# Performance work log

Measured on AMD Instinct MI355X. Metric: run time of the kernel, lower is better.

Reference implementation:

```python
import jax, jax.numpy as jnp
import numpy as np

C = 1024
CI = 256  # in_channels // inter_ratio
BN_EPS = 1e-5


def setup_inputs() -> dict:
    key = jax.random.key(0)
    ks = jax.random.split(key, 12)
    B, H, W = 16, 64, 32
    xavier = lambda k, o, i: jax.random.uniform(k, (o, i), jnp.float32,
                                                -np.sqrt(6.0 / (o + i)), np.sqrt(6.0 / (o + i)))
    return {
        "x": jax.random.normal(ks[0], (B, C, H, W), jnp.float32),
        "theta_w": xavier(ks[1], CI, C), "theta_b": jnp.zeros((CI,), jnp.float32),
        "phi_w": xavier(ks[2], CI, C), "phi_b": jnp.zeros((CI,), jnp.float32),
        "g_w": xavier(ks[3], CI, C), "g_b": jnp.zeros((CI,), jnp.float32),
        "w_w": xavier(ks[4], C, CI), "w_b": jnp.zeros((C,), jnp.float32),
        # BatchNorm (inference-mode) params; random (not zero-init) so the block is non-trivial
        "bn_gamma": jax.random.normal(ks[5], (C,), jnp.float32) * 0.1 + 1.0,
        "bn_beta": jax.random.normal(ks[6], (C,), jnp.float32) * 0.1,
        "bn_mean": jax.random.normal(ks[7], (C,), jnp.float32) * 0.1,
        "bn_var": jax.random.uniform(ks[8], (C,), jnp.float32, 0.5, 1.5),
    }


def reference(x, theta_w, theta_b, phi_w, phi_b, g_w, g_b, w_w, w_b,
              bn_gamma, bn_beta, bn_mean, bn_var):
    B, Cc, H, W = x.shape
    N = H * W
    xf = x.reshape(B, Cc, N)  # [B, C, N]
    # 1x1 convs == channel GEMMs
    theta = jnp.einsum('oc,bcn->bno', theta_w, xf) + theta_b  # [B, N, Ci]
    phi = jnp.einsum('oc,bcn->bon', phi_w, xf) + phi_b[:, None]  # [B, Ci, N]
    g = jnp.einsum('oc,bcn->bno', g_w, xf) + g_b  # [B, N, Ci]
    attn = jax.nn.softmax(jnp.einsum('bno,bom->bnm', theta, phi), axis=-1)  # [B, N, N]
    y = jnp.einsum('bnm,bmo->bno', attn, g)  # [B, N, Ci]
    z = jnp.einsum('co,bno->bcn', w_w, y) + w_b[None, :, None]  # [B, C, N]
    inv = bn_gamma / jnp.sqrt(bn_var + BN_EPS)
    z = (z - bn_mean[None, :, None]) * inv[None, :, None] + bn_beta[None, :, None]
    return z.reshape(B, Cc, H, W) + x
```

## Files before the change

### kernel.cpp

```cpp
#include <hip/hip_runtime.h>
#include <cstdint>

#define BATCH 16
#define CH 1024
#define CIN 256
#define NSP 2048
#define BN_EPS 1e-5f

typedef _Float16 f16;
typedef f16   f16x4 __attribute__((ext_vector_type(4)));
typedef f16   f16x8 __attribute__((ext_vector_type(8)));
typedef float f32x4 __attribute__((ext_vector_type(4)));
typedef float f32x16 __attribute__((ext_vector_type(16)));

typedef __attribute__((address_space(3))) void lds_t;
typedef __attribute__((address_space(1))) const void gbl_t;

__device__ __forceinline__ void gld16(void* l, const void* g) {
    __builtin_amdgcn_global_load_lds((gbl_t*)g, (lds_t*)l, 16, 0, 0);
}

__global__ __launch_bounds__(256) void k_prep(
    const float* __restrict__ tw, const float* __restrict__ pw,
    const float* __restrict__ gw, const float* __restrict__ ww,
    const float* __restrict__ wb, const float* __restrict__ gamma,
    const float* __restrict__ beta, const float* __restrict__ mean,
    const float* __restrict__ var,
    f16* __restrict__ w_all, float* __restrict__ inv_out, float* __restrict__ off_out)
{
    int id = blockIdx.x * 256 + threadIdx.x;
    if (id < 4 * 262144) {
        int sel = id >> 18, off = id & 262143;
        const float* src = sel == 0 ? tw : sel == 1 ? pw : sel == 2 ? gw : ww;
        w_all[id] = (f16)src[off];
    } else {
        int c = id - 4 * 262144;
        if (c < CH) {
            float iv = gamma[c] * rsqrtf(var[c] + BN_EPS);
            inv_out[c] = iv;
            off_out[c] = (wb[c] - mean[c]) * iv + beta[c];
        }
    }
}

__global__ __launch_bounds__(256) void k_transpose_x(
    const float* __restrict__ x, f16* __restrict__ xT)
{
    __shared__ float tile[64 * 65];
    int t = threadIdx.x;
    int n0 = blockIdx.x * 64, c0 = blockIdx.y * 64, b = blockIdx.z;
    const float* xb = x + (size_t)b * CH * NSP;
    for (int k = 0; k < 4; ++k) {
        int id = t + 256 * k;
        int row = id >> 4, cc = id & 15;
        float4 v = *(const float4*)(xb + (size_t)(c0 + row) * NSP + n0 + cc * 4);
        tile[row * 65 + cc * 4 + 0] = v.x;
        tile[row * 65 + cc * 4 + 1] = v.y;
        tile[row * 65 + cc * 4 + 2] = v.z;
        tile[row * 65 + cc * 4 + 3] = v.w;
    }
    __syncthreads();
    f16* xTb = xT + (size_t)b * NSP * CH;
    for (int k = 0; k < 2; ++k) {
        int id = t + 256 * k;
        int n = id >> 3, c8 = id & 7;
        f16x8 o;
        #pragma unroll
        for (int j = 0; j < 8; ++j) o[j] = (f16)tile[(c8 * 8 + j) * 65 + n];
        *(f16x8*)(xTb + (size_t)(n0 + n) * CH + c0 + c8 * 8) = o;
    }
}

__global__ __launch_bounds__(256, 3) void k_qkv(
    const f16* __restrict__ xT, const f16* __restrict__ w_all,
    const float* __restrict__ tb, const float* __restrict__ pb,
    const float* __restrict__ gb,
    f16* __restrict__ theta, f16* __restrict__ phiT, f16* __restrict__ gT)
{
    __shared__ char smem[40960];
    f16* a_lds = (f16*)smem;
    f16* b_lds = (f16*)(smem + 8192);
    int t = threadIdx.x;
    int w = t >> 6, lane = t & 63, l15 = lane & 15, q = lane >> 4;
    int sw = l15 & 7;
    int n0 = blockIdx.x * 64, b = blockIdx.y, set = blockIdx.z;
    const f16* W  = w_all + (size_t)set * (CIN * CH);
    const f16* xA = xT + ((size_t)b * NSP + n0) * CH;

    int rA  = lane >> 3;
    int ccs = (lane & 7) ^ rA;

    f32x4 acc[4][4];
    #pragma unroll
    for (int i = 0; i < 4; ++i)
        #pragma unroll
        for (int j = 0; j < 4; ++j) acc[i][j] = (f32x4){0.f, 0.f, 0.f, 0.f};

    for (int it = 0; it < 16; ++it) {
        #pragma unroll
        for (int i = 0; i < 2; ++i) {
            int win = w * 2 + i;
            int n = win * 8 + rA;
            gld16((char*)a_lds + win * 1024,
                  xA + (size_t)n * CH + it * 64 + ccs * 8);
        }
        #pragma unroll
        for (int i = 0; i < 8; ++i) {
            int win = w * 8 + i;
            int o = win * 8 + rA;
            gld16((char*)b_lds + win * 1024,
                  W + (size_t)o * CH + it * 64 + ccs * 8);
        }
        __syncthreads();

        #pragma unroll
        for (int kl = 0; kl < 2; ++kl) {
            int c16 = kl * 4 + q;
            int pos = (c16 ^ sw) & 7;
            f16x8 af[4], bfr[4];
            #pragma unroll
            for (int tn = 0; tn < 4; ++tn)
                af[tn] = *(const f16x8*)(a_lds + (16 * tn + l15) * 64 + pos * 8);
            #pragma unroll
            for (int to = 0; to < 4; ++to)
                bfr[to] = *(const f16x8*)(b_lds + (64 * w + 16 * to + l15) * 64 + pos * 8);
            #pragma unroll
            for (int tn = 0; tn < 4; ++tn)
                #pragma unroll
                for (int to = 0; to < 4; ++to)
                    acc[tn][to] = __builtin_amdgcn_mfma_f32_16x16x32_f16(
                        af[tn], bfr[to], acc[tn][to], 0, 0, 0);
        }
        __syncthreads();
    }

    const float* bias = set == 0 ? tb : set == 1 ? pb : gb;
    float bv[4];
    #pragma unroll
    for (int to = 0; to < 4; ++to) bv[to] = bias[64 * w + 16 * to + l15];

    if (set < 2) {
        f16* e_lds = (f16*)smem;
        #pragma unroll
        for (int tn = 0; tn < 4; ++tn)
            #pragma unroll
            for (int to = 0; to < 4; ++to)
                #pragma unroll
                for (int r = 0; r < 4; ++r)
                    e_lds[(16 * tn + 4 * q + r) * 256 + 64 * w + 16 * to + l15] =
                        (f16)(acc[tn][to][r] + bv[to]);
        __syncthreads();
        f16* dst = (set == 0 ? theta : phiT) + ((size_t)b * NSP + n0) * CIN;
        for (int k2 = 0; k2 < 8; ++k2) {
            int id = t + 256 * k2;
            *(f16x8*)(dst + id * 8) = *(const f16x8*)(e_lds + id * 8);
        }
    } else {
        f16* e_lds = (f16*)smem;
        #pragma unroll
        for (int tn = 0; tn < 4; ++tn)
            #pragma unroll
            for (int to = 0; to < 4; ++to)
                #pragma unroll
                for (int r = 0; r < 4; ++r)
                    e_lds[(64 * w + 16 * to + l15) * 72 + 16 * tn + 4 * q + r] =
                        (f16)(acc[tn][to][r] + bv[to]);
        __syncthreads();
        f16* dst = gT + (size_t)b * CIN * NSP + n0;
        for (int k2 = 0; k2 < 8; ++k2) {
            int id = t + 256 * k2;
            int o = id >> 3, cc = id & 7;
            *(f16x8*)(dst + (size_t)o * NSP + cc * 8) = *(const f16x8*)(e_lds + o * 72 + cc * 8);
        }
    }
}

__global__ __launch_bounds__(256, 2) void k_attn(
    const f16* __restrict__ theta, const f16* __restrict__ phiT,
    const f16* __restrict__ gT, f16* __restrict__ y)
{
    __shared__ char smem[76032];
    f16* phi_lds = (f16*)smem;
    f16* g_lds   = (f16*)(smem + 32768);
    f16* p_lds   = (f16*)(smem + 65536);
    float* pmax_lds  = (float*)(smem + 74752);
    float* psum_lds  = (float*)(smem + 75264);
    float* alpha_lds = (float*)(smem + 75776);

    int t = threadIdx.x;
    int w = t >> 6, lane = t & 63;
    int l31 = lane & 31, hi = lane >> 5;
    int qh = w & 1, kh = w >> 1;
    int b = blockIdx.x, n0 = blockIdx.y * 64;

    const f16* thb  = theta + (size_t)b * NSP * CIN;
    const f16* phib = phiT + (size_t)b * NSP * CIN;
    const f16* gTb  = gT + (size_t)b * CIN * NSP;

    f16x8 th[16];
    {
        const f16* tp = thb + (size_t)(n0 + qh * 32 + l31) * CIN + 8 * hi;
        #pragma unroll
        for (int s = 0; s < 16; ++s) th[s] = *(const f16x8*)(tp + s * 16);
    }

    f32x16 acc[2][2];
    #pragma unroll
    for (int i = 0; i < 2; ++i)
        #pragma unroll
        for (int j = 0; j < 2; ++j)
            #pragma unroll
            for (int r = 0; r < 16; ++r) acc[i][j][r] = 0.f;
    float m_run = -INFINITY, l_run = 0.f;

    int p_cdst = lane & 31;
    int g_rin = lane >> 3, g_cdst = lane & 7;
    int gc8 = t & 7, grb = t >> 3;

    #define DMA_PHI(IT)                                                         \
        _Pragma("unroll")                                                       \
        for (int i_ = 0; i_ < 8; ++i_) {                                        \
            int win_ = w * 8 + i_;                                              \
            int row_ = win_ * 2 + hi;                                           \
            int cs_ = (p_cdst & 24) | ((p_cdst ^ row_) & 7);                    \
            gld16((char*)phi_lds + win_ * 1024,                                 \
                  phib + (size_t)((IT) * 64 + row_) * CIN + cs_ * 8);           \
        }
    #define DMA_G0()                                                            \
        _Pragma("unroll")                                                       \
        for (int i_ = 0; i_ < 8; ++i_) {                                        \
            int win_ = w * 8 + i_;                                              \
            int row_ = win_ * 8 + g_rin;                                        \
            int cs_ = g_cdst ^ (row_ & 7);                                      \
            gld16((char*)g_lds + win_ * 1024,                                   \
                  gTb + (size_t)row_ * NSP + cs_ * 8);                          \
        }

    DMA_PHI(0)
    DMA_G0()
    asm volatile("s_waitcnt vmcnt(0)" ::: "memory");
    __builtin_amdgcn_s_barrier();

    int srow = kh * 32 + l31;
    int qrow = qh * 32 + l31;
    int mli  = kh * 64 + qrow;

    f16x8 gr[8];

    for (int it = 0; it < 32; ++it) {
        if (it < 31) {
            #pragma unroll
            for (int j = 0; j < 8; ++j)
                gr[j] = *(const f16x8*)(gTb + (size_t)(grb + 32 * j) * NSP
                                        + (it + 1) * 64 + gc8 * 8);
        }
        __builtin_amdgcn_sched_barrier(0);

        f32x16 s0, s1;
        #pragma unroll
        for (int r = 0; r < 16; ++r) { s0[r] = 0.f; s1[r] = 0.f; }
        __builtin_amdgcn_s_setprio(1);
        #pragma unroll
        for (int s = 0; s < 8; ++s) {
            int ch0 = 2 * s + hi;
            int sl0 = (ch0 & 24) | ((ch0 ^ srow) & 7);
            f16x8 a0 = *(const f16x8*)(phi_lds + srow * 256 + sl0 * 8);
            s0 = __builtin_amdgcn_mfma_f32_32x32x16_f16(a0, th[s], s0, 0, 0, 0);
            int ch1 = 2 * (s + 8) + hi;
            int sl1 = (ch1 & 24) | ((ch1 ^ srow) & 7);
            f16x8 a1 = *(const f16x8*)(phi_lds + srow * 256 + sl1 * 8);
            s1 = __builtin_amdgcn_mfma_f32_32x32x16_f16(a1, th[s + 8], s1, 0, 0, 0);
        }
        __builtin_amdgcn_s_setprio(0);
        f32x16 sacc = s0 + s1;

        float tmax = sacc[0];
        #pragma unroll
        for (int r = 1; r < 16; ++r) tmax = fmaxf(tmax, sacc[r]);
        tmax = fmaxf(tmax, __shfl_xor(tmax, 32));
        if (lane < 32) pmax_lds[mli] = tmax;
        asm volatile("s_waitcnt lgkmcnt(0)" ::: "memory");
        __builtin_amdgcn_s_barrier();

        if (it < 31) DMA_PHI(it + 1)

        float tile_max = fmaxf(tmax, pmax_lds[mli ^ 64]);
        float mnew  = fmaxf(m_run, tile_max);
        float alpha = __expf(m_run - mnew);
        m_run = mnew;
        float rs = 0.f;
        float pv[16];
        #pragma unroll
        for (int r = 0; r < 16; ++r) {
            pv[r] = __expf(sacc[r] - mnew);
            rs += pv[r];
        }
        rs += __shfl_xor(rs, 32);
        if (lane < 32) {
            psum_lds[mli] = rs;
            if (kh == 0) alpha_lds[qrow] = alpha;
        }
        #pragma unroll
        for (int g4 = 0; g4 < 4; ++g4) {
            f16x4 pk = { (f16)pv[4*g4+0], (f16)pv[4*g4+1], (f16)pv[4*g4+2], (f16)pv[4*g4+3] };
            *(f16x4*)(p_lds + qrow * 72 + kh * 32 + 8 * g4 + 4 * hi) = pk;
        }
        asm volatile("s_waitcnt lgkmcnt(0)" ::: "memory");
        __builtin_amdgcn_s_barrier();

        l_run = l_run * alpha + rs + psum_lds[mli ^ 64];

        f32x4 av[2][4];
        float mn = 1.0f;
        #pragma unroll
        for (int Mt = 0; Mt < 2; ++Mt)
            #pragma unroll
            for (int g4 = 0; g4 < 4; ++g4) {
                av[Mt][g4] = *(const f32x4*)(alpha_lds + Mt * 32 + 8 * g4 + 4 * hi);
                mn = fminf(mn, fminf(fminf(av[Mt][g4][0], av[Mt][g4][1]),
                                     fminf(av[Mt][g4][2], av[Mt][g4][3])));
            }
        if (__any(mn < 1.0f)) {
            #pragma unroll
            for (int Mt = 0; Mt < 2; ++Mt)
                #pragma unroll
                for (int g4 = 0; g4 < 4; ++g4)
                    #pragma unroll
                    for (int rr = 0; rr < 4; ++rr) {
                        acc[Mt][0][4*g4+rr] *= av[Mt][g4][rr];
                        acc[Mt][1][4*g4+rr] *= av[Mt][g4][rr];
                    }
        }

        __builtin_amdgcn_s_setprio(1);
        #pragma unroll
        for (int ks = 0; ks < 4; ++ks) {
            f16x8 pa0 = *(const f16x8*)(p_lds + l31 * 72 + ks * 16 + 8 * hi);
            f16x8 pa1 = *(const f16x8*)(p_lds + (32 + l31) * 72 + ks * 16 + 8 * hi);
            int slot = (2 * ks + hi) ^ (l31 & 7);
            f16x8 gb0 = *(const f16x8*)(g_lds + (64 * w + l31) * 64 + slot * 8);
            f16x8 gb1 = *(const f16x8*)(g_lds + (64 * w + 32 + l31) * 64 + slot * 8);
            acc[0][0] = __builtin_amdgcn_mfma_f32_32x32x16_f16(pa0, gb0, acc[0][0], 0, 0, 0);
            acc[0][1] = __builtin_amdgcn_mfma_f32_32x32x16_f16(pa0, gb1, acc[0][1], 0, 0, 0);
            acc[1][0] = __builtin_amdgcn_mfma_f32_32x32x16_f16(pa1, gb0, acc[1][0], 0, 0, 0);
            acc[1][1] = __builtin_amdgcn_mfma_f32_32x32x16_f16(pa1, gb1, acc[1][1], 0, 0, 0);
        }
        __builtin_amdgcn_s_setprio(0);
        asm volatile("s_waitcnt lgkmcnt(0)" ::: "memory");
        __builtin_amdgcn_s_barrier();

        if (it < 31) {
            asm volatile("s_waitcnt vmcnt(8)" ::: "memory");
            #pragma unroll
            for (int j = 0; j < 8; ++j) {
                int o = grb + 32 * j;
                *(f16x8*)(g_lds + o * 64 + (gc8 ^ (o & 7)) * 8) = gr[j];
            }
            asm volatile("s_waitcnt vmcnt(0) lgkmcnt(0)" ::: "memory");
            __builtin_amdgcn_s_barrier();
        }
    }

    if (lane < 32 && kh == 0) alpha_lds[qrow] = 1.0f / l_run;
    __syncthreads();
    f16* e_lds = (f16*)smem;
    #pragma unroll
    for (int Mt = 0; Mt < 2; ++Mt)
        #pragma unroll
        for (int g4 = 0; g4 < 4; ++g4) {
            f32x4 lv = *(const f32x4*)(alpha_lds + Mt * 32 + 8 * g4 + 4 * hi);
            #pragma unroll
            for (int rr = 0; rr < 4; ++rr) {
                int q = Mt * 32 + 8 * g4 + 4 * hi + rr;
                #pragma unroll
                for (int Nt = 0; Nt < 2; ++Nt) {
                    int cin = 64 * w + Nt * 32 + l31;
                    e_lds[q * 264 + cin] = (f16)(acc[Mt][Nt][4*g4+rr] * lv[rr]);
                }
            }
        }
    __syncthreads();
    f16* dst = y + ((size_t)b * NSP + n0) * CIN;
    for (int k2 = 0; k2 < 8; ++k2) {
        int id = t + 256 * k2;
        int row = id >> 5, cc = id & 31;
        *(f16x8*)(dst + (size_t)row * CIN + cc * 8) = *(const f16x8*)(e_lds + row * 264 + cc * 8);
    }
    #undef DMA_PHI
    #undef DMA_G0
}

__global__ __launch_bounds__(256, 3) void k_out(
    const f16* __restrict__ yv, const f16* __restrict__ ww,
    const float* __restrict__ inv, const float* __restrict__ off,
    const float* __restrict__ x, float* __restrict__ out)
{
    __shared__ char smem[40960];
    f16*   a_lds = (f16*)smem;
    f16*   b_lds = (f16*)(smem + 8192);
    float* z_lds = (float*)smem;
    int t = threadIdx.x;
    int w = t >> 6, lane = t & 63, l15 = lane & 15, q = lane >> 4;
    int sw = l15 & 7;
    int n0 = blockIdx.x * 64, cb = blockIdx.y * 256, b = blockIdx.z;

    const f16* yA = yv + ((size_t)b * NSP + n0) * CIN;
    const f16* W  = ww + (size_t)cb * CIN;

    int rA  = lane >> 3;
    int ccs = (lane & 7) ^ rA;

    f32x4 acc[4][4];
    #pragma unroll
    for (int i = 0; i < 4; ++i)
        #pragma unroll
        for (int j = 0; j < 4; ++j) acc[i][j] = (f32x4){0.f, 0.f, 0.f, 0.f};

    for (int it = 0; it < 4; ++it) {
        #pragma unroll
        for (int i = 0; i < 2; ++i) {
            int win = w * 2 + i;
            int n = win * 8 + rA;
            gld16((char*)a_lds + win * 1024,
                  yA + (size_t)n * CIN + it * 64 + ccs * 8);
        }
        #pragma unroll
        for (int i = 0; i < 8; ++i) {
            int win = w * 8 + i;
            int o = win * 8 + rA;
            gld16((char*)b_lds + win * 1024,
                  W + (size_t)o * CIN + it * 64 + ccs * 8);
        }
        __syncthreads();

        #pragma unroll
        for (int kl = 0; kl < 2; ++kl) {
            int c16 = kl * 4 + q;
            int pos = (c16 ^ sw) & 7;
            f16x8 af[4], bfr[4];
            #pragma unroll
            for (int tn = 0; tn < 4; ++tn)
                af[tn] = *(const f16x8*)(a_lds + (16 * tn + l15) * 64 + pos * 8);
            #pragma unroll
            for (int to = 0; to < 4; ++to)
                bfr[to] = *(const f16x8*)(b_lds + (64 * w + 16 * to + l15) * 64 + pos * 8);
            #pragma unroll
            for (int tn = 0; tn < 4; ++tn)
                #pragma unroll
                for (int to = 0; to < 4; ++to)
                    acc[tn][to] = __builtin_amdgcn_mfma_f32_16x16x32_f16(
                        af[tn], bfr[to], acc[tn][to], 0, 0, 0);
        }
        __syncthreads();
    }

    float4 xv[4];
    #pragma unroll
    for (int k2 = 0; k2 < 4; ++k2) {
        int f = t + 256 * k2;
        int zrr = f >> 4, nn4 = f & 15;
        int c = cb + 64 * (zrr >> 4) + (zrr & 15);
        xv[k2] = *(const float4*)(x + ((size_t)b * CH + c) * NSP + n0 + nn4 * 4);
    }

    #pragma unroll
    for (int to = 0; to < 4; ++to) {
        #pragma unroll
        for (int tn = 0; tn < 4; ++tn)
            #pragma unroll
            for (int r = 0; r < 4; ++r)
                z_lds[(16 * w + l15) * 68 + 16 * tn + 4 * q + r] = acc[tn][to][r];
        __syncthreads();

        float4 nxt[4];
        if (to < 3) {
            #pragma unroll
            for (int k2 = 0; k2 < 4; ++k2) {
                int f = t + 256 * k2;
                int zrr = f >> 4, nn4 = f & 15;
                int c = cb + 64 * (zrr >> 4) + 16 * (to + 1) + (zrr & 15);
                nxt[k2] = *(const float4*)(x + ((size_t)b * CH + c) * NSP + n0 + nn4 * 4);
            }
        }

        #pragma unroll
        for (int k2 = 0; k2 < 4; ++k2) {
            int f = t + 256 * k2;
            int zrr = f >> 4, nn4 = f & 15;
            int c = cb + 64 * (zrr >> 4) + 16 * to + (zrr & 15);
            float4 z = *(const float4*)(z_lds + zrr * 68 + nn4 * 4);
            float iv = inv[c], ov = off[c];
            size_t idx = ((size_t)b * CH + c) * NSP + n0 + nn4 * 4;
            float4 o;
            o.x = z.x * iv + ov + xv[k2].x;
            o.y = z.y * iv + ov + xv[k2].y;
            o.z = z.z * iv + ov + xv[k2].z;
            o.w = z.w * iv + ov + xv[k2].w;
            *(float4*)(out + idx) = o;
        }

        if (to < 3) {
            #pragma unroll
            for (int k2 = 0; k2 < 4; ++k2) xv[k2] = nxt[k2];
            __syncthreads();
        }
    }
}

extern "C" void kernel_launch(void* const* d_in, const int* in_sizes, int n_in,
                              void* d_out, int out_size, void* d_ws, size_t ws_size,
                              hipStream_t stream)
{
    const float* x     = (const float*)d_in[0];
    const float* tw    = (const float*)d_in[1];
    const float* tb    = (const float*)d_in[2];
    const float* pw    = (const float*)d_in[3];
    const float* pb    = (const float*)d_in[4];
    const float* gw    = (const float*)d_in[5];
    const float* gb_   = (const float*)d_in[6];
    const float* ww    = (const float*)d_in[7];
    const float* wb    = (const float*)d_in[8];
    const float* gamma = (const float*)d_in[9];
    const float* beta  = (const float*)d_in[10];
    const float* mean  = (const float*)d_in[11];
    const float* var   = (const float*)d_in[12];
    float* out = (float*)d_out;

    char* ws = (char*)d_ws;
    f16* xT    = (f16*)ws;
    f16* theta = (f16*)(ws + 67108864);
    f16* phiT  = (f16*)(ws + 83886080);
    f16* gT    = (f16*)(ws + 100663296);
    f16* yv    = (f16*)(ws + 117440512);
    f16* w_all = (f16*)(ws + 134217728);
    float* inv  = (float*)(ws + 136314880);
    float* offv = (float*)(ws + 136318976);

    k_prep<<<4100, 256, 0, stream>>>(tw, pw, gw, ww, wb, gamma, beta, mean, var,
                                     w_all, inv, offv);
    k_transpose_x<<<dim3(32, 16, 16), 256, 0, stream>>>(x, xT);
    k_qkv<<<dim3(32, 16, 3), 256, 0, stream>>>(xT, w_all, tb, pb, gb_, theta, phiT, gT);
    k_attn<<<dim3(16, 32), 256, 0, stream>>>(theta, phiT, gT, yv);
    k_out<<<dim3(32, 4, 16), 256, 0, stream>>>(yv, w_all + 3 * 262144, inv, offv, x, out);
}
```

Measured before the change: 471.2 us.

## Use lazy softmax rescaling, per-wave g tile ownership, and drop a barrier

The softmax running max is now updated only when a tile's max exceeds it by more than 8 (lazy rescaling), and a shared LDS flag tells waves whether to rescale the accumulators. This replaces the per-lane alpha scan and vote. The g tile is now loaded into LDS by the wave that consumes it, in padded rows (stride 68) instead of XOR-swizzled ones. That ownership lets the barrier between the PV MFMAs and the g refill be removed. The P buffer stride becomes 76 and the max and sum reductions become trees. Lazy rescaling lets unnormalized exponentials grow up to e^8 in fp16, which risks precision loss, and the flag and barrier ordering must stay correct.

```diff
diff --git a/kernel.cpp b/kernel.cpp
--- a/kernel.cpp
+++ b/kernel.cpp
@@ -179,13 +179,14 @@
     const f16* __restrict__ theta, const f16* __restrict__ phiT,
     const f16* __restrict__ gT, f16* __restrict__ y)
 {
-    __shared__ char smem[76032];
+    __shared__ char smem[78720];
     f16* phi_lds = (f16*)smem;
     f16* g_lds   = (f16*)(smem + 32768);
-    f16* p_lds   = (f16*)(smem + 65536);
-    float* pmax_lds  = (float*)(smem + 74752);
-    float* psum_lds  = (float*)(smem + 75264);
-    float* alpha_lds = (float*)(smem + 75776);
+    f16* p_lds   = (f16*)(smem + 67584);
+    float* pmax_lds  = (float*)(smem + 77312);
+    float* psum_lds  = (float*)(smem + 77824);
+    float* alpha_lds = (float*)(smem + 78336);
+    int*   flag_lds  = (int*)(smem + 78592);
 
     int t = threadIdx.x;
     int w = t >> 6, lane = t & 63;
@@ -214,8 +215,7 @@
     float m_run = -INFINITY, l_run = 0.f;
 
     int p_cdst = lane & 31;
-    int g_rin = lane >> 3, g_cdst = lane & 7;
-    int gc8 = t & 7, grb = t >> 3;
+    int g_r8 = lane >> 3, g_c8 = lane & 7;
 
     #define DMA_PHI(IT)                                                         \
         _Pragma("unroll")                                                       \
@@ -226,33 +226,31 @@
             gld16((char*)phi_lds + win_ * 1024,                                 \
                   phib + (size_t)((IT) * 64 + row_) * CIN + cs_ * 8);           \
         }
-    #define DMA_G0()                                                            \
-        _Pragma("unroll")                                                       \
-        for (int i_ = 0; i_ < 8; ++i_) {                                        \
-            int win_ = w * 8 + i_;                                              \
-            int row_ = win_ * 8 + g_rin;                                        \
-            int cs_ = g_cdst ^ (row_ & 7);                                      \
-            gld16((char*)g_lds + win_ * 1024,                                   \
-                  gTb + (size_t)row_ * NSP + cs_ * 8);                          \
-        }
-
+
+    f16x8 gr[8];
+    #pragma unroll
+    for (int j = 0; j < 8; ++j)
+        gr[j] = *(const f16x8*)(gTb + (size_t)(64 * w + 8 * j + g_r8) * NSP + g_c8 * 8);
     DMA_PHI(0)
-    DMA_G0()
-    asm volatile("s_waitcnt vmcnt(0)" ::: "memory");
+    asm volatile("s_waitcnt vmcnt(8)" ::: "memory");
+    #pragma unroll
+    for (int j = 0; j < 8; ++j)
+        *(f16x8*)(g_lds + (64 * w + 8 * j + g_r8) * 68 + g_c8 * 8) = gr[j];
+    if (t == 0) flag_lds[0] = 0;
+    asm volatile("s_waitcnt vmcnt(0) lgkmcnt(0)" ::: "memory");
     __builtin_amdgcn_s_barrier();
+    __builtin_amdgcn_sched_barrier(0);
 
     int srow = kh * 32 + l31;
     int qrow = qh * 32 + l31;
     int mli  = kh * 64 + qrow;
 
-    f16x8 gr[8];
-
     for (int it = 0; it < 32; ++it) {
         if (it < 31) {
             #pragma unroll
             for (int j = 0; j < 8; ++j)
-                gr[j] = *(const f16x8*)(gTb + (size_t)(grb + 32 * j) * NSP
-                                        + (it + 1) * 64 + gc8 * 8);
+                gr[j] = *(const f16x8*)(gTb + (size_t)(64 * w + 8 * j + g_r8) * NSP
+                                        + (it + 1) * 64 + g_c8 * 8);
         }
         __builtin_amdgcn_sched_barrier(0);
 
@@ -274,93 +272,95 @@
         __builtin_amdgcn_s_setprio(0);
         f32x16 sacc = s0 + s1;
 
-        float tmax = sacc[0];
-        #pragma unroll
-        for (int r = 1; r < 16; ++r) tmax = fmaxf(tmax, sacc[r]);
+        float m01 = fmaxf(sacc[0], sacc[1]),  m23 = fmaxf(sacc[2], sacc[3]);
+        float m45 = fmaxf(sacc[4], sacc[5]),  m67 = fmaxf(sacc[6], sacc[7]);
+        float m89 = fmaxf(sacc[8], sacc[9]),  mab = fmaxf(sacc[10], sacc[11]);
+        float mcd = fmaxf(sacc[12], sacc[13]), mef = fmaxf(sacc[14], sacc[15]);
+        float tmax = fmaxf(fmaxf(fmaxf(m01, m23), fmaxf(m45, m67)),
+                           fmaxf(fmaxf(m89, mab), fmaxf(mcd, mef)));
         tmax = fmaxf(tmax, __shfl_xor(tmax, 32));
         if (lane < 32) pmax_lds[mli] = tmax;
         asm volatile("s_waitcnt lgkmcnt(0)" ::: "memory");
         __builtin_amdgcn_s_barrier();
+        __builtin_amdgcn_sched_barrier(0);
 
         if (it < 31) DMA_PHI(it + 1)
 
         float tile_max = fmaxf(tmax, pmax_lds[mli ^ 64]);
-        float mnew  = fmaxf(m_run, tile_max);
-        float alpha = __expf(m_run - mnew);
+        bool need = tile_max > m_run + 8.0f;
+        float mnew  = need ? fmaxf(m_run, tile_max) : m_run;
+        float alpha = need ? __expf(m_run - mnew) : 1.0f;
         m_run = mnew;
+        float pv[16];
+        #pragma unroll
+        for (int r = 0; r < 16; ++r) pv[r] = __expf(sacc[r] - mnew);
         float rs = 0.f;
-        float pv[16];
-        #pragma unroll
-        for (int r = 0; r < 16; ++r) {
-            pv[r] = __expf(sacc[r] - mnew);
-            rs += pv[r];
+        {
+            float a01 = pv[0]+pv[1], a23 = pv[2]+pv[3], a45 = pv[4]+pv[5], a67 = pv[6]+pv[7];
+            float a89 = pv[8]+pv[9], aab = pv[10]+pv[11], acd = pv[12]+pv[13], aef = pv[14]+pv[15];
+            rs = ((a01+a23)+(a45+a67)) + ((a89+aab)+(acd+aef));
         }
         rs += __shfl_xor(rs, 32);
         if (lane < 32) {
             psum_lds[mli] = rs;
             if (kh == 0) alpha_lds[qrow] = alpha;
         }
+        if (need) flag_lds[0] = 1;
         #pragma unroll
         for (int g4 = 0; g4 < 4; ++g4) {
             f16x4 pk = { (f16)pv[4*g4+0], (f16)pv[4*g4+1], (f16)pv[4*g4+2], (f16)pv[4*g4+3] };
-            *(f16x4*)(p_lds + qrow * 72 + kh * 32 + 8 * g4 + 4 * hi) = pk;
+            *(f16x4*)(p_lds + qrow * 76 + kh * 32 + 8 * g4 + 4 * hi) = pk;
         }
         asm volatile("s_waitcnt lgkmcnt(0)" ::: "memory");
         __builtin_amdgcn_s_barrier();
+        __builtin_amdgcn_sched_barrier(0);
 
         l_run = l_run * alpha + rs + psum_lds[mli ^ 64];
 
-        f32x4 av[2][4];
-        float mn = 1.0f;
-        #pragma unroll
-        for (int Mt = 0; Mt < 2; ++Mt)
-            #pragma unroll
-            for (int g4 = 0; g4 < 4; ++g4) {
-                av[Mt][g4] = *(const f32x4*)(alpha_lds + Mt * 32 + 8 * g4 + 4 * hi);
-                mn = fminf(mn, fminf(fminf(av[Mt][g4][0], av[Mt][g4][1]),
-                                     fminf(av[Mt][g4][2], av[Mt][g4][3])));
-            }
-        if (__any(mn < 1.0f)) {
+        if (flag_lds[0]) {
             #pragma unroll
             for (int Mt = 0; Mt < 2; ++Mt)
                 #pragma unroll
-                for (int g4 = 0; g4 < 4; ++g4)
+                for (int g4 = 0; g4 < 4; ++g4) {
+                    f32x4 av = *(const f32x4*)(alpha_lds + Mt * 32 + 8 * g4 + 4 * hi);
                     #pragma unroll
                     for (int rr = 0; rr < 4; ++rr) {
-                        acc[Mt][0][4*g4+rr] *= av[Mt][g4][rr];
-                        acc[Mt][1][4*g4+rr] *= av[Mt][g4][rr];
+                        acc[Mt][0][4*g4+rr] *= av[rr];
+                        acc[Mt][1][4*g4+rr] *= av[rr];
                     }
+                }
         }
 
         __builtin_amdgcn_s_setprio(1);
         #pragma unroll
         for (int ks = 0; ks < 4; ++ks) {
-            f16x8 pa0 = *(const f16x8*)(p_lds + l31 * 72 + ks * 16 + 8 * hi);
-            f16x8 pa1 = *(const f16x8*)(p_lds + (32 + l31) * 72 + ks * 16 + 8 * hi);
-            int slot = (2 * ks + hi) ^ (l31 & 7);
-            f16x8 gb0 = *(const f16x8*)(g_lds + (64 * w + l31) * 64 + slot * 8);
-            f16x8 gb1 = *(const f16x8*)(g_lds + (64 * w + 32 + l31) * 64 + slot * 8);
+            f16x8 pa0 = *(const f16x8*)(p_lds + l31 * 76 + ks * 16 + 8 * hi);
+            f16x8 pa1 = *(const f16x8*)(p_lds + (32 + l31) * 76 + ks * 16 + 8 * hi);
+            f16x8 gb0 = *(const f16x8*)(g_lds + (64 * w + l31) * 68 + ks * 16 + 8 * hi);
+            f16x8 gb1 = *(const f16x8*)(g_lds + (64 * w + 32 + l31) * 68 + ks * 16 + 8 * hi);
             acc[0][0] = __builtin_amdgcn_mfma_f32_32x32x16_f16(pa0, gb0, acc[0][0], 0, 0, 0);
             acc[0][1] = __builtin_amdgcn_mfma_f32_32x32x16_f16(pa0, gb1, acc[0][1], 0, 0, 0);
             acc[1][0] = __builtin_amdgcn_mfma_f32_32x32x16_f16(pa1, gb0, acc[1][0], 0, 0, 0);
             acc[1][1] = __builtin_amdgcn_mfma_f32_32x32x16_f16(pa1, gb1, acc[1][1], 0, 0, 0);
         }
         __builtin_amdgcn_s_setprio(0);
-        asm volatile("s_waitcnt lgkmcnt(0)" ::: "memory");
-        __builtin_amdgcn_s_barrier();
 
         if (it < 31) {
+            asm volatile("s_waitcnt lgkmcnt(0)" ::: "memory");
             asm volatile("s_waitcnt vmcnt(8)" ::: "memory");
-            #pragma unroll
-            for (int j = 0; j < 8; ++j) {
-                int o = grb + 32 * j;
-                *(f16x8*)(g_lds + o * 64 + (gc8 ^ (o & 7)) * 8) = gr[j];
-            }
+            __builtin_amdgcn_sched_barrier(0);
+            #pragma unroll
+            for (int j = 0; j < 8; ++j)
+                *(f16x8*)(g_lds + (64 * w + 8 * j + g_r8) * 68 + g_c8 * 8) = gr[j];
             asm volatile("s_waitcnt vmcnt(0) lgkmcnt(0)" ::: "memory");
             __builtin_amdgcn_s_barrier();
-        }
-    }
-
+            __builtin_amdgcn_sched_barrier(0);
+            if (t == 0) flag_lds[0] = 0;
+        }
+    }
+
+    asm volatile("s_waitcnt lgkmcnt(0)" ::: "memory");
+    __builtin_amdgcn_s_barrier();
     if (lane < 32 && kh == 0) alpha_lds[qrow] = 1.0f / l_run;
     __syncthreads();
     f16* e_lds = (f16*)smem;
@@ -387,7 +387,6 @@
         *(f16x8*)(dst + (size_t)row * CIN + cc * 8) = *(const f16x8*)(e_lds + row * 264 + cc * 8);
     }
     #undef DMA_PHI
-    #undef DMA_G0
 }
 
 __global__ __launch_bounds__(256, 3) void k_out(
```

New measurement: 581.3 us. +23.4%, slower.
